# Performance work log

Hardware: AMD Instinct MI355X
Metric: run time of the kernel (lower is better)

## Reference

```python
import jax, jax.numpy as jnp
import numpy as np

EPS = 1e-12  # matches F.normalize clamp


def sparsemax(z):
    # Martins & Astudillo sparsemax along the last axis
    K = z.shape[-1]
    z_sorted = -jnp.sort(-z, axis=-1)                      # descending
    k = jnp.arange(1, K + 1, dtype=z.dtype)
    z_cum = jnp.cumsum(z_sorted, axis=-1)
    support = (1.0 + k * z_sorted) > z_cum                 # [..., K]
    k_z = jnp.sum(support, axis=-1, keepdims=True)         # support size
    tau = (jnp.take_along_axis(z_cum, k_z - 1, axis=-1) - 1.0) / k_z.astype(z.dtype)
    return jnp.maximum(z - tau, 0.0)


def setup_inputs() -> dict:
    key = jax.random.key(0)
    k1, k2, k3 = jax.random.split(key, 3)
    B, IN, OUT = 8192, 512, 4096
    x = jax.random.normal(k1, (B, IN), dtype=jnp.float32)
    weight = jax.random.normal(k2, (OUT, IN), dtype=jnp.float32)
    lambd = jnp.square(jax.random.normal(k3, (1,), dtype=jnp.float32))  # torch init: randn**2
    return {"x": x, "weight": weight, "lambd": lambd}


def reference(x, weight, lambd):
    # normalize prototypes and inputs onto the unit hypersphere
    w_n = weight / jnp.maximum(jnp.linalg.norm(weight, axis=-1, keepdims=True), EPS)
    x_n = x / jnp.maximum(jnp.linalg.norm(x, axis=1, keepdims=True), EPS)
    xa = x_n @ w_n.T                                        # [B, OUT]
    # ||x - a||^2 via Gram expansion (avoids [B, OUT, IN] broadcast tensor)
    x2 = jnp.sum(x_n * x_n, axis=-1, keepdims=True)         # [B, 1]
    w2 = jnp.sum(w_n * w_n, axis=-1)                        # [OUT]
    sq_dist = x2 + w2[None, :] - 2.0 * xa                   # [B, OUT]
    logits = xa - lambd * sq_dist                           # kds_mode='recon_dist'
    return sparsemax(logits)
```

## Files before the change

kernel.cpp:

```cpp
#include <hip/hip_runtime.h>

typedef __attribute__((ext_vector_type(8))) short bf16x8;
typedef __attribute__((ext_vector_type(4))) float f32x4;

__device__ inline unsigned short f2bf(float f) {
  union { float f; unsigned u; } v; v.f = f;
  unsigned r = v.u + 0x7FFFu + ((v.u >> 16) & 1u);
  return (unsigned short)(r >> 16);
}

__global__ __launch_bounds__(256) void normalize_both(
    const float* __restrict__ x, const float* __restrict__ wgt,
    unsigned short* __restrict__ xb, unsigned short* __restrict__ wb) {
  const int w = threadIdx.x >> 6, lane = threadIdx.x & 63;
  const int row = blockIdx.x * 4 + w;
  const float* src;
  unsigned short* dst;
  if (row < 8192) { src = x + (size_t)row * 512;           dst = xb + (size_t)row * 512; }
  else            { src = wgt + (size_t)(row - 8192) * 512; dst = wb + (size_t)(row - 8192) * 512; }
  const float* p = src + lane * 8;
  float4 a = *reinterpret_cast<const float4*>(p);
  float4 b = *reinterpret_cast<const float4*>(p + 4);
  float ss = a.x*a.x + a.y*a.y + a.z*a.z + a.w*a.w
           + b.x*b.x + b.y*b.y + b.z*b.z + b.w*b.w;
  #pragma unroll
  for (int off = 32; off; off >>= 1) ss += __shfl_xor(ss, off);
  const float inv = 1.0f / fmaxf(sqrtf(ss), 1e-12f);
  unsigned short o[8];
  o[0]=f2bf(a.x*inv); o[1]=f2bf(a.y*inv); o[2]=f2bf(a.z*inv); o[3]=f2bf(a.w*inv);
  o[4]=f2bf(b.x*inv); o[5]=f2bf(b.y*inv); o[6]=f2bf(b.z*inv); o[7]=f2bf(b.w*inv);
  *reinterpret_cast<uint4*>(dst + lane * 8) = *reinterpret_cast<uint4*>(o);
}

#define BM 256
#define BN 256
#define BK 32

#define STAGE_A(slot_, ko_, j_)                                                   \
  do {                                                                            \
    const int c_ = wid * 2 + (j_);                                                \
    const unsigned short* s_ = Xb + (size_t)(bm0 + c_ * 16 + srow) * 512 + (ko_) + sskel; \
    __builtin_amdgcn_global_load_lds(                                             \
        (const __attribute__((address_space(1))) void*)s_,                        \
        (__attribute__((address_space(3))) void*)&As[slot_][c_ * 512], 16, 0, 0); \
  } while (0)
#define STAGE_B(slot_, ko_, j_)                                                   \
  do {                                                                            \
    const int c_ = wid * 2 + (j_);                                                \
    const unsigned short* s_ = Wb + (size_t)(bn0 + c_ * 16 + srow) * 512 + (ko_) + sskel; \
    __builtin_amdgcn_global_load_lds(                                             \
        (const __attribute__((address_space(1))) void*)s_,                        \
        (__attribute__((address_space(3))) void*)&Bs[slot_][c_ * 512], 16, 0, 0); \
  } while (0)

__global__ __launch_bounds__(512, 2) void gemm_logits_f16(
    const unsigned short* __restrict__ Xb, const unsigned short* __restrict__ Wb,
    const float* __restrict__ lambd, unsigned short* __restrict__ out16) {
  __shared__ unsigned short As[3][BM * BK];
  __shared__ unsigned short Bs[3][BN * BK];
  const int tid = threadIdx.x, lane = tid & 63, wid = tid >> 6;
  const int wm = wid >> 2, wn = wid & 3;
  const int lrow = lane & 15, kg = lane >> 4;

  const int id = (int)blockIdx.x;
  const int swz = (id & 7) * 64 + (id >> 3);
  const int bx = swz & 15;
  const int by = swz >> 4;
  const int bm0 = by * BM, bn0 = bx * BN;

  const int srow  = lane >> 2;
  const int sskel = ((lane & 3) ^ ((lane >> 3) & 3)) * 8;

  const int rswz = (lrow >> 1) & 3;
  const int kA = (kg ^ rswz) * 8;

  f32x4 acc[8][4];
  #pragma unroll
  for (int m = 0; m < 8; ++m)
    #pragma unroll
    for (int n = 0; n < 4; ++n) { f32x4 z = {0.f,0.f,0.f,0.f}; acc[m][n] = z; }

  STAGE_A(0, 0, 0); STAGE_A(0, 0, 1); STAGE_B(0, 0, 0); STAGE_B(0, 0, 1);
  STAGE_A(1, BK, 0); STAGE_A(1, BK, 1); STAGE_B(1, BK, 0); STAGE_B(1, BK, 1);
  asm volatile("s_waitcnt vmcnt(4)" ::: "memory");
  asm volatile("s_barrier" ::: "memory");

  #pragma unroll
  for (int t = 0; t < 16; ++t) {
    const int cur = t % 3, nx2 = (t + 2) % 3;
    if (t + 2 < 16) {
      STAGE_A(nx2, (t + 2) * BK, 0); STAGE_A(nx2, (t + 2) * BK, 1);
      STAGE_B(nx2, (t + 2) * BK, 0); STAGE_B(nx2, (t + 2) * BK, 1);
    }
    bf16x8 af[8], bfr[4];
    #pragma unroll
    for (int fr = 0; fr < 8; ++fr)
      af[fr] = *reinterpret_cast<const bf16x8*>(
          &As[cur][(wm * 128 + fr * 16 + lrow) * BK + kA]);
    #pragma unroll
    for (int fc = 0; fc < 4; ++fc)
      bfr[fc] = *reinterpret_cast<const bf16x8*>(
          &Bs[cur][(wn * 64 + fc * 16 + lrow) * BK + kA]);
    #pragma unroll
    for (int fr = 0; fr < 8; ++fr)
      #pragma unroll
      for (int fc = 0; fc < 4; ++fc)
        acc[fr][fc] = __builtin_amdgcn_mfma_f32_16x16x32_bf16(
            bfr[fc], af[fr], acc[fr][fc], 0, 0, 0);
    if (t < 15) {
      if (t < 13) { asm volatile("s_waitcnt vmcnt(4)" ::: "memory"); }
      else        { asm volatile("s_waitcnt vmcnt(0)" ::: "memory"); }
      asm volatile("s_barrier" ::: "memory");
    }
  }

  const float lam = lambd[0];
  const float sa_ = 1.0f + 2.0f * lam, sb_ = 2.0f * lam;
  #pragma unroll
  for (int fr = 0; fr < 8; ++fr) {
    const int gr = bm0 + wm * 128 + fr * 16 + lrow;
    #pragma unroll
    for (int fc = 0; fc < 4; ++fc) {
      const int gc = bn0 + wn * 64 + fc * 16 + kg * 4;
      union { _Float16 h[2]; unsigned u; } p0, p1;
      p0.h[0] = (_Float16)(sa_ * acc[fr][fc][0] - sb_);
      p0.h[1] = (_Float16)(sa_ * acc[fr][fc][1] - sb_);
      p1.h[0] = (_Float16)(sa_ * acc[fr][fc][2] - sb_);
      p1.h[1] = (_Float16)(sa_ * acc[fr][fc][3] - sb_);
      uint2 pk; pk.x = p0.u; pk.y = p1.u;
      *reinterpret_cast<uint2*>(&out16[(size_t)gr * 4096 + gc]) = pk;
    }
  }
}

__global__ __launch_bounds__(256) void sparsemax_wave(
    const unsigned short* __restrict__ zin, float* __restrict__ out) {
  const int lane = threadIdx.x & 63;
  const int row  = ((int)blockIdx.x << 2) + (threadIdx.x >> 6);
  const unsigned short* zr = zin + (size_t)row * 4096;
  float* orow = out + (size_t)row * 4096;

  float v[64];
  #pragma unroll
  for (int c = 0; c < 8; ++c) {
    uint4 pk = *reinterpret_cast<const uint4*>(&zr[c * 512 + lane * 8]);
    const unsigned short* ph = reinterpret_cast<const unsigned short*>(&pk);
    #pragma unroll
    for (int j = 0; j < 8; ++j) {
      union { unsigned short u; _Float16 h; } cv; cv.u = ph[j];
      v[c * 8 + j] = (float)cv.h;
    }
  }

  float ls = 0.f;
  #pragma unroll
  for (int j = 0; j < 64; ++j) ls += v[j];
  #pragma unroll
  for (int off = 32; off; off >>= 1) ls += __shfl_xor(ls, off);
  float tau = (ls - 1.0f) * (1.0f / 4096.0f);
  int prevC = 4096;

  for (int it = 0; it < 32; ++it) {
    float s = 0.f; int c = 0;
    #pragma unroll
    for (int j = 0; j < 64; ++j) { if (v[j] > tau) { s += v[j]; ++c; } }
    #pragma unroll
    for (int off = 32; off; off >>= 1) { s += __shfl_xor(s, off); c += __shfl_xor(c, off); }
    tau = (s - 1.0f) / (float)c;
    if (c == prevC) break;
    prevC = c;
  }

  #pragma unroll
  for (int c = 0; c < 8; ++c) {
    float4 t0, t1;
    t0.x = fmaxf(v[c*8+0] - tau, 0.f);
    t0.y = fmaxf(v[c*8+1] - tau, 0.f);
    t0.z = fmaxf(v[c*8+2] - tau, 0.f);
    t0.w = fmaxf(v[c*8+3] - tau, 0.f);
    t1.x = fmaxf(v[c*8+4] - tau, 0.f);
    t1.y = fmaxf(v[c*8+5] - tau, 0.f);
    t1.z = fmaxf(v[c*8+6] - tau, 0.f);
    t1.w = fmaxf(v[c*8+7] - tau, 0.f);
    *reinterpret_cast<float4*>(&orow[c * 512 + lane * 8])     = t0;
    *reinterpret_cast<float4*>(&orow[c * 512 + lane * 8 + 4]) = t1;
  }
}

extern "C" void kernel_launch(void* const* d_in, const int* in_sizes, int n_in,
                              void* d_out, int out_size, void* d_ws, size_t ws_size,
                              hipStream_t stream) {
  const float* x     = (const float*)d_in[0];
  const float* wgt   = (const float*)d_in[1];
  const float* lambd = (const float*)d_in[2];
  float* out = (float*)d_out;

  unsigned short* xb  = (unsigned short*)d_ws;
  unsigned short* wb  = xb + (size_t)8192 * 512;
  unsigned short* z16 = wb + (size_t)4096 * 512;

  normalize_both<<<(8192 + 4096) / 4, 256, 0, stream>>>(x, wgt, xb, wb);

  gemm_logits_f16<<<512, 512, 0, stream>>>(xb, wb, lambd, z16);

  sparsemax_wave<<<8192 / 4, 256, 0, stream>>>(z16, out);
}
```

Measured before the change: 102.0 us.

## Split GEMM K-step into two phases with interleaved loads and MFMA priority

The GEMM main loop now runs in two halves. The first half issues the A-tile prefetch, reads half the A fragments plus the B fragments, and runs 16 MFMAs. The second half issues the B prefetch, reads the remaining A fragments, and runs the other 16 MFMAs. Scheduling barriers and s_setprio raise wave priority around the MFMA clusters, so global and LDS traffic interleaves with matrix work across the waves on a CU. This also lowers register pressure for the A fragments. In exchange it adds extra lgkmcnt waits and fixed ordering, which may serialize LDS reads against MFMAs within a wave.

```diff
diff --git a/kernel.cpp b/kernel.cpp
--- a/kernel.cpp
+++ b/kernel.cpp
@@ -83,34 +83,55 @@
   STAGE_A(0, 0, 0); STAGE_A(0, 0, 1); STAGE_B(0, 0, 0); STAGE_B(0, 0, 1);
   STAGE_A(1, BK, 0); STAGE_A(1, BK, 1); STAGE_B(1, BK, 0); STAGE_B(1, BK, 1);
   asm volatile("s_waitcnt vmcnt(4)" ::: "memory");
-  asm volatile("s_barrier" ::: "memory");
+  __builtin_amdgcn_s_barrier();
+  __builtin_amdgcn_sched_barrier(0);
 
   #pragma unroll
   for (int t = 0; t < 16; ++t) {
     const int cur = t % 3, nx2 = (t + 2) % 3;
-    if (t + 2 < 16) {
-      STAGE_A(nx2, (t + 2) * BK, 0); STAGE_A(nx2, (t + 2) * BK, 1);
-      STAGE_B(nx2, (t + 2) * BK, 0); STAGE_B(nx2, (t + 2) * BK, 1);
-    }
-    bf16x8 af[8], bfr[4];
-    #pragma unroll
-    for (int fr = 0; fr < 8; ++fr)
-      af[fr] = *reinterpret_cast<const bf16x8*>(
+    if (t + 2 < 16) { STAGE_A(nx2, (t + 2) * BK, 0); STAGE_A(nx2, (t + 2) * BK, 1); }
+    bf16x8 af0[4], bfr[4];
+    #pragma unroll
+    for (int fr = 0; fr < 4; ++fr)
+      af0[fr] = *reinterpret_cast<const bf16x8*>(
           &As[cur][(wm * 128 + fr * 16 + lrow) * BK + kA]);
     #pragma unroll
     for (int fc = 0; fc < 4; ++fc)
       bfr[fc] = *reinterpret_cast<const bf16x8*>(
           &Bs[cur][(wn * 64 + fc * 16 + lrow) * BK + kA]);
-    #pragma unroll
-    for (int fr = 0; fr < 8; ++fr)
+    asm volatile("s_waitcnt lgkmcnt(0)" ::: "memory");
+    __builtin_amdgcn_sched_barrier(0);
+    __builtin_amdgcn_s_setprio(1);
+    #pragma unroll
+    for (int fr = 0; fr < 4; ++fr)
       #pragma unroll
       for (int fc = 0; fc < 4; ++fc)
         acc[fr][fc] = __builtin_amdgcn_mfma_f32_16x16x32_bf16(
-            bfr[fc], af[fr], acc[fr][fc], 0, 0, 0);
+            bfr[fc], af0[fr], acc[fr][fc], 0, 0, 0);
+    __builtin_amdgcn_s_setprio(0);
+    __builtin_amdgcn_sched_barrier(0);
+    if (t + 2 < 16) { STAGE_B(nx2, (t + 2) * BK, 0); STAGE_B(nx2, (t + 2) * BK, 1); }
+    bf16x8 af1[4];
+    #pragma unroll
+    for (int fr = 0; fr < 4; ++fr)
+      af1[fr] = *reinterpret_cast<const bf16x8*>(
+          &As[cur][(wm * 128 + 64 + fr * 16 + lrow) * BK + kA]);
+    asm volatile("s_waitcnt lgkmcnt(0)" ::: "memory");
+    __builtin_amdgcn_sched_barrier(0);
+    __builtin_amdgcn_s_setprio(1);
+    #pragma unroll
+    for (int fr = 0; fr < 4; ++fr)
+      #pragma unroll
+      for (int fc = 0; fc < 4; ++fc)
+        acc[fr + 4][fc] = __builtin_amdgcn_mfma_f32_16x16x32_bf16(
+            bfr[fc], af1[fr], acc[fr + 4][fc], 0, 0, 0);
+    __builtin_amdgcn_s_setprio(0);
+    __builtin_amdgcn_sched_barrier(0);
     if (t < 15) {
       if (t < 13) { asm volatile("s_waitcnt vmcnt(4)" ::: "memory"); }
       else        { asm volatile("s_waitcnt vmcnt(0)" ::: "memory"); }
-      asm volatile("s_barrier" ::: "memory");
+      __builtin_amdgcn_s_barrier();
+      __builtin_amdgcn_sched_barrier(0);
     }
   }
 
```

After: 99.59 us. 2.4% less time.
